# Optimization experiments

Hardware: AMD Instinct MI355X
Metric: run time of the kernel (lower is better)

Reference implementation:

```python
import jax, jax.numpy as jnp
import numpy as np

B, T, INPUT_DIM = 32, 256, 512
VQ_DIM = 128
NUM_EMBED = 8192
CODEBOOK_NUM = 1
SPLIT_NUM = 4
FREQ = INPUT_DIM // 2 + 1  # 257


def setup_inputs() -> dict:
    key = jax.random.key(0)
    k1, k2, k3, k4 = jax.random.split(key, 4)
    x = jax.random.normal(k1, (B, T, INPUT_DIM), dtype=jnp.float32)
    # xavier_normal_ on (input_dim, vq_dim): std = sqrt(2/(fan_in+fan_out))
    xav_std = float(np.sqrt(2.0 / (INPUT_DIM + VQ_DIM)))
    projector = jax.random.normal(k2, (INPUT_DIM, VQ_DIM), dtype=jnp.float32) * xav_std
    codebook = jax.random.normal(k3, (CODEBOOK_NUM, NUM_EMBED, VQ_DIM), dtype=jnp.float32)
    random_matrix = jax.random.randint(k4, (FREQ,), 0, SPLIT_NUM, dtype=jnp.int32)
    return {"x": x, "projector": projector, "codebook": codebook,
            "random_matrix": random_matrix}


def reference(x, projector, codebook, random_matrix):
    n = x.shape[-1]
    x_fft = jnp.fft.rfft(x, axis=-1)                              # [B,T,F] complex
    # masks[s, f] = (random_matrix[f] == s); vectorizes the per-split list
    masks = (random_matrix[None, :] == jnp.arange(SPLIT_NUM)[:, None])  # [S,F] bool
    x_sub = x_fft[:, :, None, :] * masks                           # [B,T,S,F]
    x_recon = jnp.fft.irfft(x_sub, n=n, axis=-1)                   # [B,T,S,n]
    feat = jnp.einsum('btns,sd->btnd', x_recon, projector)         # [B,T,S,D]
    feat = feat / jnp.linalg.norm(feat, axis=-1, keepdims=True)
    cb = codebook / jnp.linalg.norm(codebook, axis=-1, keepdims=True)  # [C,M,D]
    sim = jnp.einsum('btnd,cmd->btncm', feat, cb)                  # [B,T,S,C,M]
    return jnp.argmax(sim, axis=-1)                                # [B,T,S,C]
```

## Files before the change

kernel.cpp:

```cpp
#include <hip/hip_runtime.h>
#include <math.h>

#define BT 8192
#define NDIM 512
#define NFREQ 257
#define DDIM 128
#define NEMBED 8192
#define NQ 4
#define ROWS 32768

typedef _Float16 half8 __attribute__((ext_vector_type(8)));
typedef _Float16 half2v __attribute__((ext_vector_type(2)));
typedef float f32x4 __attribute__((ext_vector_type(4)));

#define SCALE_DN 2.44140625e-4f

__global__ __launch_bounds__(512) void build_K_kernel(const int* __restrict__ rm,
                                                      float* __restrict__ Kmat) {
    __shared__ float ctab[512];
    __shared__ int rms[NFREQ];
    int t = threadIdx.x;
    ctab[t] = cospif((float)t * (1.0f / 256.0f));
    if (t < NFREQ) rms[t] = rm[t];
    __syncthreads();
    float acc0 = 0.f, acc1 = 0.f, acc2 = 0.f, acc3 = 0.f;
    for (int f = 0; f < NFREQ; ++f) {
        float w = (f == 0 || f == 256) ? 1.0f : 2.0f;
        float c = w * ctab[(f * t) & 511];
        int s = rms[f];
        acc0 += (s == 0) ? c : 0.0f;
        acc1 += (s == 1) ? c : 0.0f;
        acc2 += (s == 2) ? c : 0.0f;
        acc3 += (s == 3) ? c : 0.0f;
    }
    const float sc = 1.0f / 512.0f;
    Kmat[0 * 512 + t] = acc0 * sc;
    Kmat[1 * 512 + t] = acc1 * sc;
    Kmat[2 * 512 + t] = acc2 * sc;
    Kmat[3 * 512 + t] = acc3 * sc;
}

__global__ __launch_bounds__(128) void build_W_split(const float* __restrict__ proj,
                                                     const float* __restrict__ Kmat,
                                                     _Float16* __restrict__ Wth,
                                                     _Float16* __restrict__ Wtl) {
    int nt = blockIdx.x, s = blockIdx.y, d = threadIdx.x;
    int n0 = nt * 8;
    __shared__ float Ks[512];
    for (int i = d; i < 512; i += 128) Ks[i] = Kmat[s * 512 + i];
    __syncthreads();
    float acc[8] = {};
    for (int p16 = 0; p16 < 512; p16 += 16) {
        float wv[23];
#pragma unroll
        for (int j2 = 0; j2 < 23; ++j2) wv[j2] = Ks[(p16 - n0 + j2 - 7) & 511];
#pragma unroll
        for (int j = 0; j < 16; ++j) {
            float xp = proj[(p16 + j) * DDIM + d];
#pragma unroll
            for (int i = 0; i < 8; ++i)
                acc[i] = fmaf(xp, wv[7 + j - i], acc[i]);
        }
    }
    size_t cbase = (size_t)(s * DDIM + d) * 512 + n0;
#pragma unroll
    for (int i = 0; i < 8; ++i) {
        float f = acc[i] * 256.0f;
        _Float16 h = (_Float16)f;
        Wth[cbase + i] = h;
        Wtl[cbase + i] = (_Float16)((f - (float)h) * 4096.0f);
    }
}

__global__ __launch_bounds__(256) void cbsplit_kernel(const float* __restrict__ cb,
                                                      _Float16* __restrict__ chi,
                                                      _Float16* __restrict__ clo) {
    int code = blockIdx.x * 4 + (threadIdx.x >> 6);
    int l = threadIdx.x & 63;
    float2 v = ((const float2*)(cb + (size_t)code * DDIM))[l];
    float ss = fmaf(v.x, v.x, v.y * v.y);
#pragma unroll
    for (int m = 32; m; m >>= 1) ss += __shfl_xor(ss, m);
    float r = 1.0f / sqrtf(ss);
    float a = v.x * r, b = v.y * r;
    _Float16 ha = (_Float16)a, hb = (_Float16)b;
    half2v hv = {ha, hb};
    half2v lv = {(_Float16)((a - (float)ha) * 4096.0f), (_Float16)((b - (float)hb) * 4096.0f)};
    int row = code & 15, tile = code >> 4;
    int cp = (l >> 2) ^ (row & 7);
    size_t base = (size_t)tile * 2048 + row * 128 + cp * 8 + (l & 3) * 2;
    *(half2v*)(chi + base) = hv;
    *(half2v*)(clo + base) = lv;
}

__global__ __launch_bounds__(256) void fused_feat(const float* __restrict__ x,
                                                  const _Float16* __restrict__ Wth,
                                                  const _Float16* __restrict__ Wtl,
                                                  _Float16* __restrict__ fhi,
                                                  _Float16* __restrict__ flo) {
    __shared__ __align__(16) char smem[59392];
    float* xs = (float*)smem;
    _Float16* Wh = (_Float16*)(smem + 18432);
    _Float16* Wl = (_Float16*)(smem + 38912);

    int t = threadIdx.x;
    int w = t >> 6, lr = t & 15, lg = (t >> 4) & 3;
    int row0 = blockIdx.x * 64;
    int sIdx = blockIdx.y;

    int xr_r = t >> 2, xr_c = (t & 3) * 8;
    int wcol = t >> 1, wh_h = t & 1;
    const float* xsrc = x + (size_t)(row0 + xr_r) * NDIM + xr_c;
    const _Float16* whsrc = Wth + (size_t)(sIdx * 128 + wcol) * 512 + wh_h * 16;
    const _Float16* wlsrc = Wtl + (size_t)(sIdx * 128 + wcol) * 512 + wh_h * 16;

    f32x4 c0[8], c1[8];
#pragma unroll
    for (int i = 0; i < 8; ++i) { c0[i] = (f32x4){0.f,0.f,0.f,0.f}; c1[i] = c0[i]; }

    {
        float4 a0 = *(const float4*)(xsrc);
        float4 a1 = *(const float4*)(xsrc + 4);
        *(float4*)&xs[xr_r * 36 + xr_c] = a0;
        *(float4*)&xs[xr_r * 36 + xr_c + 4] = a1;
        half8 h0 = *(const half8*)(whsrc);
        half8 h1 = *(const half8*)(whsrc + 8);
        half8 l0 = *(const half8*)(wlsrc);
        half8 l1 = *(const half8*)(wlsrc + 8);
        *(half8*)&Wh[wcol * 40 + wh_h * 16] = h0;
        *(half8*)&Wh[wcol * 40 + wh_h * 16 + 8] = h1;
        *(half8*)&Wl[wcol * 40 + wh_h * 16] = l0;
        *(half8*)&Wl[wcol * 40 + wh_h * 16 + 8] = l1;
    }

    for (int it = 0; it < 16; ++it) {
        __syncthreads();
        int buf = it & 1;
        float4 nx0, nx1; half8 nh0, nh1, nl0, nl1;
        bool have = (it + 1) < 16;
        if (have) {
            int k0 = (it + 1) * 32;
            nx0 = *(const float4*)(xsrc + k0);
            nx1 = *(const float4*)(xsrc + k0 + 4);
            nh0 = *(const half8*)(whsrc + k0);
            nh1 = *(const half8*)(whsrc + k0 + 8);
            nl0 = *(const half8*)(wlsrc + k0);
            nl1 = *(const half8*)(wlsrc + k0 + 8);
        }
        const float* xb = xs + buf * 2304;
        float4 f0 = *(const float4*)&xb[(w * 16 + lr) * 36 + lg * 8];
        float4 f1 = *(const float4*)&xb[(w * 16 + lr) * 36 + lg * 8 + 4];
        float fv[8] = {f0.x, f0.y, f0.z, f0.w, f1.x, f1.y, f1.z, f1.w};
        half8 ah, al;
#pragma unroll
        for (int j = 0; j < 8; ++j) {
            _Float16 h = (_Float16)fv[j];
            ah[j] = h;
            al[j] = (_Float16)((fv[j] - (float)h) * 4096.0f);
        }
        const _Float16* whb = Wh + buf * 5120;
        const _Float16* wlb = Wl + buf * 5120;
#pragma unroll
        for (int set = 0; set < 8; ++set) {
            int bcol = set * 16 + lr;
            half8 bh = *(const half8*)&whb[bcol * 40 + lg * 8];
            half8 bl = *(const half8*)&wlb[bcol * 40 + lg * 8];
            c0[set] = __builtin_amdgcn_mfma_f32_16x16x32_f16(ah, bh, c0[set], 0, 0, 0);
            c1[set] = __builtin_amdgcn_mfma_f32_16x16x32_f16(ah, bl, c1[set], 0, 0, 0);
            c1[set] = __builtin_amdgcn_mfma_f32_16x16x32_f16(al, bh, c1[set], 0, 0, 0);
        }
        __syncthreads();
        if (have) {
            *(float4*)&xs[(buf ^ 1) * 2304 + xr_r * 36 + xr_c] = nx0;
            *(float4*)&xs[(buf ^ 1) * 2304 + xr_r * 36 + xr_c + 4] = nx1;
            _Float16* dh = Wh + (buf ^ 1) * 5120 + wcol * 40 + wh_h * 16;
            _Float16* dl = Wl + (buf ^ 1) * 5120 + wcol * 40 + wh_h * 16;
            *(half8*)(dh) = nh0; *(half8*)(dh + 8) = nh1;
            *(half8*)(dl) = nl0; *(half8*)(dl + 8) = nl1;
        }
    }
    __syncthreads();

    float* few = (float*)smem + w * 2112;
    float ss[4] = {0.f, 0.f, 0.f, 0.f};
    float vv[8][4];
#pragma unroll
    for (int set = 0; set < 8; ++set)
#pragma unroll
        for (int r = 0; r < 4; ++r) {
            float v = fmaf(c1[set][r], SCALE_DN, c0[set][r]);
            vv[set][r] = v;
            ss[r] = fmaf(v, v, ss[r]);
        }
#pragma unroll
    for (int r = 0; r < 4; ++r) {
#pragma unroll
        for (int m = 1; m < 16; m <<= 1) ss[r] += __shfl_xor(ss[r], m);
    }
    float rn[4];
#pragma unroll
    for (int r = 0; r < 4; ++r) rn[r] = rsqrtf(ss[r]);
#pragma unroll
    for (int set = 0; set < 8; ++set)
#pragma unroll
        for (int r = 0; r < 4; ++r)
            few[(4 * lg + r) * 132 + set * 16 + lr] = vv[set][r] * rn[r];
    __syncthreads();
    int l = t & 63;
    int rr = l >> 2, q = l & 3;
    size_t btg = (size_t)(row0 + w * 16 + rr);
    size_t dst = (btg * 4 + sIdx) * DDIM + q * 32;
#pragma unroll
    for (int g = 0; g < 4; ++g) {
        half8 oh, ol;
#pragma unroll
        for (int j = 0; j < 8; ++j) {
            float f = few[rr * 132 + q * 32 + g * 8 + j];
            _Float16 h = (_Float16)f;
            oh[j] = h;
            ol[j] = (_Float16)((f - (float)h) * 4096.0f);
        }
        *(half8*)(fhi + dst + g * 8) = oh;
        *(half8*)(flo + dst + g * 8) = ol;
    }
}

__global__ __launch_bounds__(256, 2) void sim_argmax_part(const _Float16* __restrict__ fhi,
                                                          const _Float16* __restrict__ flo,
                                                          const _Float16* __restrict__ chi,
                                                          const _Float16* __restrict__ clo,
                                                          float* __restrict__ pv,
                                                          int* __restrict__ pi) {
    __shared__ _Float16 Bh[2][2048];
    __shared__ _Float16 Bl[2][2048];
    __shared__ float redv[256][17];
    __shared__ int   redi[256][17];

    int t = threadIdx.x;
    int w = t >> 6, lr = t & 15, lg = (t >> 4) & 3;
    int row0 = blockIdx.x * 256;
    int q = blockIdx.y;

    half8 ahi[4][4], alo[4][4];
#pragma unroll
    for (int s = 0; s < 4; ++s)
#pragma unroll
        for (int kt = 0; kt < 4; ++kt) {
            size_t off = (size_t)(row0 + w * 64 + s * 16 + lr) * DDIM + kt * 32 + lg * 8;
            ahi[s][kt] = *(const half8*)(fhi + off);
            alo[s][kt] = *(const half8*)(flo + off);
        }

    int roff[4];
#pragma unroll
    for (int kt = 0; kt < 4; ++kt)
        roff[kt] = lr * 128 + (((kt << 2) | lg) ^ (lr & 7)) * 8;

    const half8* chv = (const half8*)chi + (size_t)q * 32768;
    const half8* clv = (const half8*)clo + (size_t)q * 32768;

    float best[4][4];
    int btile[4][4];
#pragma unroll
    for (int s = 0; s < 4; ++s)
#pragma unroll
        for (int r = 0; r < 4; ++r) { best[s][r] = -1e30f; btile[s][r] = 0; }

    *(half8*)&Bh[0][t * 8] = chv[t];
    *(half8*)&Bl[0][t * 8] = clv[t];

    const int NT = NEMBED / (16 * NQ);
    for (int it = 0; it < NT; ++it) {
        __syncthreads();
        int buf = it & 1;
        half8 nh, nl;
        bool have = (it + 1) < NT;
        if (have) {
            nh = chv[(it + 1) * 256 + t];
            nl = clv[(it + 1) * 256 + t];
        }
        f32x4 a0[4], a1[4];
#pragma unroll
        for (int s = 0; s < 4; ++s) { a0[s] = (f32x4){0.f,0.f,0.f,0.f}; a1[s] = a0[s]; }
#pragma unroll
        for (int kt = 0; kt < 4; ++kt) {
            half8 bh = *(const half8*)&Bh[buf][roff[kt]];
            half8 bl = *(const half8*)&Bl[buf][roff[kt]];
#pragma unroll
            for (int s = 0; s < 4; ++s) {
                a0[s] = __builtin_amdgcn_mfma_f32_16x16x32_f16(ahi[s][kt], bh, a0[s], 0, 0, 0);
                a1[s] = __builtin_amdgcn_mfma_f32_16x16x32_f16(ahi[s][kt], bl, a1[s], 0, 0, 0);
                a1[s] = __builtin_amdgcn_mfma_f32_16x16x32_f16(alo[s][kt], bh, a1[s], 0, 0, 0);
            }
        }
#pragma unroll
        for (int s = 0; s < 4; ++s)
#pragma unroll
            for (int r = 0; r < 4; ++r) {
                float v = fmaf(a1[s][r], SCALE_DN, a0[s][r]);
                if (v > best[s][r]) { best[s][r] = v; btile[s][r] = it; }
            }
        if (have) {
            *(half8*)&Bh[buf ^ 1][t * 8] = nh;
            *(half8*)&Bl[buf ^ 1][t * 8] = nl;
        }
    }

#pragma unroll
    for (int s = 0; s < 4; ++s)
#pragma unroll
        for (int r = 0; r < 4; ++r) {
            int row = w * 64 + s * 16 + 4 * lg + r;
            redv[row][lr] = best[s][r];
            redi[row][lr] = q * (NEMBED / NQ) + btile[s][r] * 16 + lr;
        }
    __syncthreads();
    {
        float bv = redv[t][0]; int bi = redi[t][0];
#pragma unroll
        for (int c = 1; c < 16; ++c) {
            float v = redv[t][c]; int ii = redi[t][c];
            if (v > bv || (v == bv && ii < bi)) { bv = v; bi = ii; }
        }
        pv[(size_t)q * ROWS + row0 + t] = bv;
        pi[(size_t)q * ROWS + row0 + t] = bi;
    }
}

__global__ __launch_bounds__(256) void merge_argmax(const float* __restrict__ pv,
                                                    const int* __restrict__ pi,
                                                    int* __restrict__ out) {
    int row = blockIdx.x * 256 + threadIdx.x;
    float bv = pv[row]; int bi = pi[row];
#pragma unroll
    for (int q = 1; q < NQ; ++q) {
        float v = pv[(size_t)q * ROWS + row];
        if (v > bv) { bv = v; bi = pi[(size_t)q * ROWS + row]; }
    }
    out[row] = bi;
}

extern "C" void kernel_launch(void* const* d_in, const int* in_sizes, int n_in,
                              void* d_out, int out_size, void* d_ws, size_t ws_size,
                              hipStream_t stream) {
    const float* x    = (const float*)d_in[0];
    const float* proj = (const float*)d_in[1];
    const float* cb   = (const float*)d_in[2];
    const int*   rm   = (const int*)d_in[3];
    int* out = (int*)d_out;

    char* wsb = (char*)d_ws;
    float*    Kmat = (float*)(wsb + 0);
    _Float16* Wth  = (_Float16*)(wsb + 8192);
    _Float16* Wtl  = (_Float16*)(wsb + 532480);
    _Float16* chi  = (_Float16*)(wsb + 1056768);
    _Float16* clo  = (_Float16*)(wsb + 3153920);
    _Float16* fhi  = (_Float16*)(wsb + 5251072);
    _Float16* flo  = (_Float16*)(wsb + 13639680);
    float*    pv   = (float*)(wsb + 22028288);
    int*      pi   = (int*)(wsb + 22552576);

    build_K_kernel<<<1, 512, 0, stream>>>(rm, Kmat);
    build_W_split<<<dim3(64, 4), 128, 0, stream>>>(proj, Kmat, Wth, Wtl);
    cbsplit_kernel<<<NEMBED / 4, 256, 0, stream>>>(cb, chi, clo);
    fused_feat<<<dim3(128, 4), 256, 0, stream>>>(x, Wth, Wtl, fhi, flo);
    sim_argmax_part<<<dim3(ROWS / 256, NQ), 256, 0, stream>>>(fhi, flo, chi, clo, pv, pi);
    merge_argmax<<<ROWS / 256, 256, 0, stream>>>(pv, pi, out);
}
```

Baseline: 300.1 us.

## Load codebook MFMA fragments directly from global into registers, drop LDS staging

The codebook split kernel now writes hi/lo halves in an MFMA-fragment-ordered layout, so each lane's B operand is one contiguous half8 per k-step. The sim kernel then loads those fragments straight from global memory (L2-shared across waves) into registers and prefetches the next tile per k-step. This removes the LDS double buffer and the per-iteration __syncthreads. In exchange, every wave issues its own global loads for the same codebook tile (4x redundant traffic served from cache), and memory latency is exposed if the prefetch does not cover it.

```diff
diff --git a/kernel.cpp b/kernel.cpp
--- a/kernel.cpp
+++ b/kernel.cpp
@@ -86,11 +86,11 @@
     _Float16 ha = (_Float16)a, hb = (_Float16)b;
     half2v hv = {ha, hb};
     half2v lv = {(_Float16)((a - (float)ha) * 4096.0f), (_Float16)((b - (float)hb) * 4096.0f)};
-    int row = code & 15, tile = code >> 4;
-    int cp = (l >> 2) ^ (row & 7);
-    size_t base = (size_t)tile * 2048 + row * 128 + cp * 8 + (l & 3) * 2;
-    *(half2v*)(chi + base) = hv;
-    *(half2v*)(clo + base) = lv;
+    int cr = code & 15, tile = code >> 4;
+    int kt = l >> 4, lg = (l >> 2) & 3, j = 2 * (l & 3);
+    size_t addr = (size_t)tile * 2048 + kt * 512 + lg * 128 + cr * 8 + j;
+    *(half2v*)(chi + addr) = hv;
+    *(half2v*)(clo + addr) = lv;
 }
 
 __global__ __launch_bounds__(256) void fused_feat(const float* __restrict__ x,
@@ -231,13 +231,11 @@
                                                           const _Float16* __restrict__ clo,
                                                           float* __restrict__ pv,
                                                           int* __restrict__ pi) {
-    __shared__ _Float16 Bh[2][2048];
-    __shared__ _Float16 Bl[2][2048];
     __shared__ float redv[256][17];
     __shared__ int   redi[256][17];
 
     int t = threadIdx.x;
-    int w = t >> 6, lr = t & 15, lg = (t >> 4) & 3;
+    int w = t >> 6, l = t & 63, lr = t & 15, lg = (t >> 4) & 3;
     int row0 = blockIdx.x * 256;
     int q = blockIdx.y;
 
@@ -251,13 +249,16 @@
             alo[s][kt] = *(const half8*)(flo + off);
         }
 
-    int roff[4];
-#pragma unroll
-    for (int kt = 0; kt < 4; ++kt)
-        roff[kt] = lr * 128 + (((kt << 2) | lg) ^ (lr & 7)) * 8;
-
-    const half8* chv = (const half8*)chi + (size_t)q * 32768;
-    const half8* clv = (const half8*)clo + (size_t)q * 32768;
+    const half8* cf = (const half8*)chi;
+    const half8* cv = (const half8*)clo;
+    size_t base = (size_t)(q * (NEMBED / NQ / 16)) * 256 + l;
+
+    half8 bh[4], bl[4];
+#pragma unroll
+    for (int kt = 0; kt < 4; ++kt) {
+        bh[kt] = cf[base + kt * 64];
+        bl[kt] = cv[base + kt * 64];
+    }
 
     float best[4][4];
     int btile[4][4];
@@ -266,31 +267,24 @@
 #pragma unroll
         for (int r = 0; r < 4; ++r) { best[s][r] = -1e30f; btile[s][r] = 0; }
 
-    *(half8*)&Bh[0][t * 8] = chv[t];
-    *(half8*)&Bl[0][t * 8] = clv[t];
-
     const int NT = NEMBED / (16 * NQ);
     for (int it = 0; it < NT; ++it) {
-        __syncthreads();
-        int buf = it & 1;
-        half8 nh, nl;
+        f32x4 a0[4], a1[4];
+#pragma unroll
+        for (int s = 0; s < 4; ++s) { a0[s] = (f32x4){0.f,0.f,0.f,0.f}; a1[s] = a0[s]; }
+        size_t nb = base + (size_t)(it + 1) * 256;
         bool have = (it + 1) < NT;
-        if (have) {
-            nh = chv[(it + 1) * 256 + t];
-            nl = clv[(it + 1) * 256 + t];
-        }
-        f32x4 a0[4], a1[4];
-#pragma unroll
-        for (int s = 0; s < 4; ++s) { a0[s] = (f32x4){0.f,0.f,0.f,0.f}; a1[s] = a0[s]; }
 #pragma unroll
         for (int kt = 0; kt < 4; ++kt) {
-            half8 bh = *(const half8*)&Bh[buf][roff[kt]];
-            half8 bl = *(const half8*)&Bl[buf][roff[kt]];
 #pragma unroll
             for (int s = 0; s < 4; ++s) {
-                a0[s] = __builtin_amdgcn_mfma_f32_16x16x32_f16(ahi[s][kt], bh, a0[s], 0, 0, 0);
-                a1[s] = __builtin_amdgcn_mfma_f32_16x16x32_f16(ahi[s][kt], bl, a1[s], 0, 0, 0);
-                a1[s] = __builtin_amdgcn_mfma_f32_16x16x32_f16(alo[s][kt], bh, a1[s], 0, 0, 0);
+                a0[s] = __builtin_amdgcn_mfma_f32_16x16x32_f16(ahi[s][kt], bh[kt], a0[s], 0, 0, 0);
+                a1[s] = __builtin_amdgcn_mfma_f32_16x16x32_f16(ahi[s][kt], bl[kt], a1[s], 0, 0, 0);
+                a1[s] = __builtin_amdgcn_mfma_f32_16x16x32_f16(alo[s][kt], bh[kt], a1[s], 0, 0, 0);
+            }
+            if (have) {
+                bh[kt] = cf[nb + kt * 64];
+                bl[kt] = cv[nb + kt * 64];
             }
         }
 #pragma unroll
@@ -300,10 +294,6 @@
                 float v = fmaf(a1[s][r], SCALE_DN, a0[s][r]);
                 if (v > best[s][r]) { best[s][r] = v; btile[s][r] = it; }
             }
-        if (have) {
-            *(half8*)&Bh[buf ^ 1][t * 8] = nh;
-            *(half8*)&Bl[buf ^ 1][t * 8] = nl;
-        }
     }
 
 #pragma unroll
```

Measured after the change: 285.0 us. 1.05x faster.
